# Optimization experiments

Hardware: AMD Instinct MI355X
Metric: run time of the kernel (lower is better)

The kernel has to match this reference:

```python
import jax, jax.numpy as jnp
import numpy as np

EMBED_DIM = 1024
NUM_HEADS = 16
HEAD_DIM = EMBED_DIM // NUM_HEADS
BATCH = 2
SEQ = 2048


def setup_inputs() -> dict:
    key = jax.random.key(0)
    k_x, k_wi, k_bi, k_wo, k_bo = jax.random.split(key, 5)
    scale_in = 1.0 / np.sqrt(EMBED_DIM)
    x = jax.random.normal(k_x, (BATCH, SEQ, EMBED_DIM), dtype=jnp.float32)
    # nn.Linear stores weight [out, in]; we keep [in, out] for x @ W.
    w_in = jax.random.uniform(k_wi, (EMBED_DIM, 3 * EMBED_DIM), jnp.float32, -scale_in, scale_in)
    b_in = jax.random.uniform(k_bi, (3 * EMBED_DIM,), jnp.float32, -scale_in, scale_in)
    w_out = jax.random.uniform(k_wo, (EMBED_DIM, EMBED_DIM), jnp.float32, -scale_in, scale_in)
    b_out = jax.random.uniform(k_bo, (EMBED_DIM,), jnp.float32, -scale_in, scale_in)
    return {"x": x, "w_in": w_in, "b_in": b_in, "w_out": w_out, "b_out": b_out}


def reference(x, w_in, b_in, w_out, b_out):
    B, S, E = x.shape
    H, D = NUM_HEADS, HEAD_DIM
    inp = x @ w_in + b_in                       # [B,S,3E]
    que, key, val = jnp.split(inp, 3, axis=-1)  # each [B,S,E]
    que = que.reshape(B, S, H, D)
    key = key.reshape(B, S, H, D)
    val = val.reshape(B, S, H, D)
    scores = jnp.einsum('bshd,brhd->bhsr', que, key) * (1.0 / np.sqrt(D))
    weights = jax.nn.softmax(scores, axis=-1)   # [B,H,S,S]
    attn = jnp.einsum('bhsr,brhd->bshd', weights, val).reshape(B, S, E)
    return attn @ w_out + b_out
```

## Files before the change

kernel.cpp:

```cpp
#include <hip/hip_runtime.h>


typedef __bf16 bf16x8 __attribute__((ext_vector_type(8)));
typedef float  f32x4  __attribute__((ext_vector_type(4)));
typedef float  f32x16 __attribute__((ext_vector_type(16)));
typedef short  s16x4  __attribute__((ext_vector_type(4)));
typedef short  s16x8  __attribute__((ext_vector_type(8)));

__device__ __forceinline__ unsigned short f2b(float f) {
  unsigned u = __float_as_uint(f);
  unsigned r = u + 0x7fffu + ((u >> 16) & 1u);
  return (unsigned short)(r >> 16);
}

__device__ __forceinline__ unsigned cvt_pk_bf16(float a, float b) {
#if defined(__HIP_DEVICE_COMPILE__)
  unsigned r;
  asm("v_cvt_pk_bf16_f32 %0, %1, %2" : "=v"(r) : "v"(a), "v"(b));
  return r;
#else
  return (unsigned)f2b(a) | ((unsigned)f2b(b) << 16);
#endif
}

__device__ __forceinline__ void permlane32_swap(unsigned& a, unsigned& b) {
#if defined(__HIP_DEVICE_COMPILE__)
  asm("v_permlane32_swap_b32 %0, %1" : "+v"(a), "+v"(b));
#endif
}

__device__ __forceinline__ void gl_lds16(const void* g, void* l) {
  __builtin_amdgcn_global_load_lds(
      (__attribute__((address_space(1))) void*)g,
      (__attribute__((address_space(3))) void*)l, 16, 0, 0);
}

__device__ __forceinline__ void transpose_cast_body(
    const float* __restrict__ in, unsigned short* __restrict__ out,
    int R, int C, int bx, int by, int tid, float tile[64][65]) {
  int r0 = by * 64, c0 = bx * 64;
#pragma unroll
  for (int p = 0; p < 16; p++) {
    int i = tid + p * 256;
    int ri = i >> 6, ci = i & 63;
    tile[ri][ci] = in[(size_t)(r0 + ri) * C + c0 + ci];
  }
  __syncthreads();
#pragma unroll
  for (int p = 0; p < 16; p++) {
    int i = tid + p * 256;
    int ci = i >> 6, ri = i & 63;
    out[(size_t)(c0 + ci) * R + r0 + ri] = f2b(tile[ri][ci]);
  }
}

__global__ __launch_bounds__(256) void prep_kernel(
    const float* __restrict__ x, unsigned short* __restrict__ xb,
    const float* __restrict__ w_in, unsigned short* __restrict__ wint,
    const float* __restrict__ w_out, unsigned short* __restrict__ woutt) {
  __shared__ float tile[64][65];
  int bid = blockIdx.x, tid = threadIdx.x;
  if (bid < 4096) {
    int i = bid * 256 + tid;
    float4 v = ((const float4*)x)[i];
    ushort4 o;
    o.x = f2b(v.x); o.y = f2b(v.y); o.z = f2b(v.z); o.w = f2b(v.w);
    ((ushort4*)xb)[i] = o;
  } else if (bid < 4864) {
    int l = bid - 4096;
    transpose_cast_body(w_in, wint, 1024, 3072, l % 48, l / 48, tid, tile);
  } else {
    int l = bid - 4864;
    transpose_cast_body(w_out, woutt, 1024, 1024, l % 16, l / 16, tid, tile);
  }
}

__global__ __launch_bounds__(256) void vt_transpose_kernel(
    const unsigned short* __restrict__ qkv, unsigned short* __restrict__ vt) {
  __shared__ unsigned short tile[64][65];
  int bid = blockIdx.x;
  int st = bid & 31, h = (bid >> 5) & 15, b = bid >> 9;
  int s0 = st * 64;
  int tid = threadIdx.x;
  const unsigned short* src = qkv + (size_t)(b * 2048 + s0) * 3072 + 2048 + h * 64;
#pragma unroll
  for (int p = 0; p < 16; p++) {
    int i = tid + p * 256;
    int sr = i >> 6, d = i & 63;
    tile[sr][d] = src[(size_t)sr * 3072 + d];
  }
  __syncthreads();
  unsigned short* dst = vt + (size_t)(b * 16 + h) * 64 * 2048 + s0;
#pragma unroll
  for (int p = 0; p < 16; p++) {
    int i = tid + p * 256;
    int dr = i >> 6, sc = i & 63;
    dst[(size_t)dr * 2048 + sc] = tile[sc][dr];
  }
}

__global__ __launch_bounds__(256) void gemm_bt1(
    const unsigned short* __restrict__ A, const unsigned short* __restrict__ Bt,
    const float* __restrict__ bias, unsigned short* __restrict__ Cp,
    int M, int N, int K, int qcols, float qscale) {
  __shared__ __align__(16) unsigned short As[128 * 32];
  __shared__ __align__(16) unsigned short Bs[128 * 32];
  int tid = threadIdx.x;
  int wave = tid >> 6, lane = tid & 63;
  int m_l = lane & 15, quad = lane >> 4;
  int wm = (wave >> 1) * 64, wn = (wave & 1) * 64;
  int row = tid >> 2, kp = (tid & 3) << 3;
  const unsigned short* ag = A + (size_t)(blockIdx.y * 128 + row) * K + kp;
  const unsigned short* bg = Bt + (size_t)(blockIdx.x * 128 + row) * K + kp;
  unsigned short* asw = As + wave * 512;
  unsigned short* bsw = Bs + wave * 512;
  f32x4 acc[4][4] = {};
  for (int k0 = 0; k0 < K; k0 += 32) {
    __syncthreads();
    gl_lds16(ag + k0, asw);
    gl_lds16(ag + (size_t)64 * K + k0, asw + 2048);
    gl_lds16(bg + k0, bsw);
    gl_lds16(bg + (size_t)64 * K + k0, bsw + 2048);
    __syncthreads();
    bf16x8 af[4], bf[4];
#pragma unroll
    for (int i = 0; i < 4; i++)
      af[i] = *(const bf16x8*)&As[(wm + i * 16 + m_l) * 32 + quad * 8];
#pragma unroll
    for (int j = 0; j < 4; j++)
      bf[j] = *(const bf16x8*)&Bs[(wn + j * 16 + m_l) * 32 + quad * 8];
#pragma unroll
    for (int i = 0; i < 4; i++)
#pragma unroll
      for (int j = 0; j < 4; j++)
        acc[i][j] = __builtin_amdgcn_mfma_f32_16x16x32_bf16(af[i], bf[j], acc[i][j], 0, 0, 0);
  }
  float bv[4];
#pragma unroll
  for (int j = 0; j < 4; j++) bv[j] = bias[blockIdx.x * 128 + wn + j * 16 + m_l];
#pragma unroll
  for (int i = 0; i < 4; i++) {
    int m = blockIdx.y * 128 + wm + i * 16 + quad * 4;
#pragma unroll
    for (int j = 0; j < 4; j++) {
      int n = blockIdx.x * 128 + wn + j * 16 + m_l;
      float sc = (n < qcols) ? qscale : 1.0f;
#pragma unroll
      for (int r = 0; r < 4; r++) {
        float v = (acc[i][j][r] + bv[j]) * sc;
        Cp[(size_t)(m + r) * N + n] = f2b(v);
      }
    }
  }
}

__global__ __launch_bounds__(256) void gemm_bt2(
    const unsigned short* __restrict__ A, const unsigned short* __restrict__ Bt,
    const float* __restrict__ bias, float* __restrict__ Cp, int M, int N, int K) {
  __shared__ __align__(16) unsigned short As[128 * 32];
  __shared__ __align__(16) unsigned short Bs[64 * 32];
  int tid = threadIdx.x;
  int wave = tid >> 6, lane = tid & 63;
  int m_l = lane & 15, quad = lane >> 4;
  int wm = (wave >> 1) * 64, wn = (wave & 1) * 32;
  int row = tid >> 2, kp = (tid & 3) << 3;
  const unsigned short* ag = A + (size_t)(blockIdx.y * 128 + row) * K + kp;
  const unsigned short* bg = Bt + (size_t)(blockIdx.x * 64 + row) * K + kp;
  unsigned short* asw = As + wave * 512;
  unsigned short* bsw = Bs + wave * 512;
  f32x4 acc[4][2] = {};
  for (int k0 = 0; k0 < K; k0 += 32) {
    __syncthreads();
    gl_lds16(ag + k0, asw);
    gl_lds16(ag + (size_t)64 * K + k0, asw + 2048);
    gl_lds16(bg + k0, bsw);
    __syncthreads();
    bf16x8 af[4], bf[2];
#pragma unroll
    for (int i = 0; i < 4; i++)
      af[i] = *(const bf16x8*)&As[(wm + i * 16 + m_l) * 32 + quad * 8];
#pragma unroll
    for (int j = 0; j < 2; j++)
      bf[j] = *(const bf16x8*)&Bs[(wn + j * 16 + m_l) * 32 + quad * 8];
#pragma unroll
    for (int i = 0; i < 4; i++)
#pragma unroll
      for (int j = 0; j < 2; j++)
        acc[i][j] = __builtin_amdgcn_mfma_f32_16x16x32_bf16(af[i], bf[j], acc[i][j], 0, 0, 0);
  }
  float bv[2];
#pragma unroll
  for (int j = 0; j < 2; j++) bv[j] = bias[blockIdx.x * 64 + wn + j * 16 + m_l];
#pragma unroll
  for (int i = 0; i < 4; i++) {
    int m = blockIdx.y * 128 + wm + i * 16 + quad * 4;
#pragma unroll
    for (int j = 0; j < 2; j++) {
      int n = blockIdx.x * 64 + wn + j * 16 + m_l;
#pragma unroll
      for (int r = 0; r < 4; r++)
        Cp[(size_t)(m + r) * N + n] = acc[i][j][r] + bv[j];
    }
  }
}

__global__ __launch_bounds__(256) void attn_kernel(
    const unsigned short* __restrict__ qkv, const unsigned short* __restrict__ vt,
    unsigned short* __restrict__ aout) {
  __shared__ __align__(16) unsigned short Qs[128 * 64];
  __shared__ __align__(16) unsigned short Ks[64 * 64];
  __shared__ __align__(16) unsigned short Vts[64 * 64];
  int bid = blockIdx.x;
  int qt = bid & 15, h = (bid >> 4) & 15, b = bid >> 8;
  int tid = threadIdx.x, wave = tid >> 6, lane = tid & 63;
  int l31 = lane & 31, hi = lane >> 5, l7 = lane & 7;
  int q0 = qt * 128;
  const unsigned short* qb = qkv + (size_t)b * 2048 * 3072 + h * 64;
  const unsigned short* kb = qb + 1024;
  const unsigned short* vtb = vt + (size_t)(b * 16 + h) * 64 * 2048;

  int srow = tid >> 3;
  int sd0 = ((tid & 7) ^ (srow & 7)) * 8;

#pragma unroll
  for (int p = 0; p < 4; p++)
    gl_lds16(qb + (size_t)(q0 + p * 32 + srow) * 3072 + sd0, Qs + p * 2048 + wave * 512);
  __syncthreads();

  bf16x8 qf[4];
  int qrow = (wave * 32 + l31) * 64;
#pragma unroll
  for (int ks = 0; ks < 4; ks++)
    qf[ks] = *(const bf16x8*)&Qs[qrow + ((2 * ks + hi) ^ l7) * 8];

  f32x16 oacc[2] = {};
  float lsum = 0.0f;

  for (int kt = 0; kt < 2048; kt += 64) {
    __syncthreads();
#pragma unroll
    for (int p = 0; p < 2; p++) {
      gl_lds16(kb + (size_t)(kt + p * 32 + srow) * 3072 + sd0, Ks + p * 2048 + wave * 512);
      gl_lds16(vtb + (size_t)(p * 32 + srow) * 2048 + kt + sd0, Vts + p * 2048 + wave * 512);
    }
    __syncthreads();

#pragma unroll
    for (int tt = 0; tt < 2; tt++) {
      f32x16 sacc = {};
#pragma unroll
      for (int ks = 0; ks < 4; ks++) {
        bf16x8 kf = *(const bf16x8*)&Ks[(tt * 32 + l31) * 64 + ((2 * ks + hi) ^ l7) * 8];
        sacc = __builtin_amdgcn_mfma_f32_32x32x16_bf16(kf, qf[ks], sacc, 0, 0, 0);
      }
      float pv[16];
#pragma unroll
      for (int i = 0; i < 16; i++) {
        pv[i] = __builtin_exp2f(sacc[i]);
        lsum += pv[i];
      }
#pragma unroll
      for (int g = 0; g < 2; g++) {
        unsigned a0 = cvt_pk_bf16(pv[8 * g + 0], pv[8 * g + 1]);
        unsigned a1 = cvt_pk_bf16(pv[8 * g + 2], pv[8 * g + 3]);
        unsigned b0 = cvt_pk_bf16(pv[8 * g + 4], pv[8 * g + 5]);
        unsigned b1 = cvt_pk_bf16(pv[8 * g + 6], pv[8 * g + 7]);
        permlane32_swap(a0, b0);
        permlane32_swap(a1, b1);
        union { unsigned u[4]; bf16x8 v; } pf;
        pf.u[0] = a0; pf.u[1] = a1; pf.u[2] = b0; pf.u[3] = b1;
        int kc = tt * 2 + g;
#pragma unroll
        for (int dt = 0; dt < 2; dt++) {
          bf16x8 vf = *(const bf16x8*)&Vts[(dt * 32 + l31) * 64 + ((kc * 2 + hi) ^ l7) * 8];
          oacc[dt] = __builtin_amdgcn_mfma_f32_32x32x16_bf16(vf, pf.v, oacc[dt], 0, 0, 0);
        }
      }
    }
  }

  float lp = lsum + __shfl_xor(lsum, 32, 64);
  float rl = 1.0f / lp;

  unsigned short* ob = aout + (size_t)(b * 2048 + q0 + wave * 32 + l31) * 1024 + h * 64;
#pragma unroll
  for (int dt = 0; dt < 2; dt++)
#pragma unroll
    for (int rq = 0; rq < 4; rq++) {
      union { uint2 u; ushort4 w; } pk;
      pk.u.x = cvt_pk_bf16(oacc[dt][4 * rq + 0] * rl, oacc[dt][4 * rq + 1] * rl);
      pk.u.y = cvt_pk_bf16(oacc[dt][4 * rq + 2] * rl, oacc[dt][4 * rq + 3] * rl);
      *(ushort4*)&ob[dt * 32 + rq * 8 + hi * 4] = pk.w;
    }
}

extern "C" void kernel_launch(void* const* d_in, const int* in_sizes, int n_in,
                              void* d_out, int out_size, void* d_ws, size_t ws_size,
                              hipStream_t stream) {
  (void)in_sizes; (void)n_in; (void)out_size; (void)ws_size;
  const float* x     = (const float*)d_in[0];
  const float* w_in  = (const float*)d_in[1];
  const float* b_in  = (const float*)d_in[2];
  const float* w_out = (const float*)d_in[3];
  const float* b_out = (const float*)d_in[4];
  char* ws = (char*)d_ws;
  unsigned short* xb    = (unsigned short*)(ws + 0);
  unsigned short* wint  = (unsigned short*)(ws + 8388608);
  unsigned short* woutt = (unsigned short*)(ws + 14680064);
  unsigned short* qkv   = (unsigned short*)(ws + 16777216);
  unsigned short* vt    = (unsigned short*)(ws + 41943040);
  unsigned short* attn  = (unsigned short*)(ws + 50331648);
  float* out = (float*)d_out;

  const float QSCALE = 0.125f * 1.44269504088896f;

  prep_kernel<<<5120, 256, 0, stream>>>(x, xb, w_in, wint, w_out, woutt);
  gemm_bt1<<<dim3(24, 32), 256, 0, stream>>>(xb, wint, b_in, qkv, 4096, 3072, 1024,
                                             1024, QSCALE);
  vt_transpose_kernel<<<1024, 256, 0, stream>>>(qkv, vt);
  attn_kernel<<<512, 256, 0, stream>>>(qkv, vt, attn);
  gemm_bt2<<<dim3(16, 32), 256, 0, stream>>>(attn, woutt, b_out, out, 4096, 1024, 1024);
}
```

Baseline: 212.8 us.

## Split attention KV loop across two wave groups with LDS reduction and MFMA row sums

The attention block grows to 512 threads. Each group of four waves handles half of every 128-key tile, which doubles the waves available to hide latency per block, and the two partial outputs are combined through LDS at the end. The row-sum of exp values is now computed by an MFMA against a ones vector instead of scalar adds. The cost is an extra reduction phase, more LDS per block, and bf16 rounding in the denominator sum.

```diff
diff --git a/kernel.cpp b/kernel.cpp
--- a/kernel.cpp
+++ b/kernel.cpp
@@ -204,16 +204,20 @@
   }
 }
 
-__global__ __launch_bounds__(256) void attn_kernel(
+__global__ __launch_bounds__(512, 4) void attn_kernel(
     const unsigned short* __restrict__ qkv, const unsigned short* __restrict__ vt,
     unsigned short* __restrict__ aout) {
-  __shared__ __align__(16) unsigned short Qs[128 * 64];
-  __shared__ __align__(16) unsigned short Ks[64 * 64];
-  __shared__ __align__(16) unsigned short Vts[64 * 64];
+  __shared__ __align__(16) unsigned short smem[24576];
+  unsigned short* Qs  = smem;
+  unsigned short* Ks  = smem + 8192;
+  unsigned short* Vts = smem + 16384;
+
   int bid = blockIdx.x;
   int qt = bid & 15, h = (bid >> 4) & 15, b = bid >> 8;
   int tid = threadIdx.x, wave = tid >> 6, lane = tid & 63;
   int l31 = lane & 31, hi = lane >> 5, l7 = lane & 7;
+  int w03 = wave & 3;
+  int koff = (wave >> 2) * 64;
   int q0 = qt * 128;
   const unsigned short* qb = qkv + (size_t)b * 2048 * 3072 + h * 64;
   const unsigned short* kb = qb + 1024;
@@ -221,28 +225,33 @@
 
   int srow = tid >> 3;
   int sd0 = ((tid & 7) ^ (srow & 7)) * 8;
-
-#pragma unroll
-  for (int p = 0; p < 4; p++)
-    gl_lds16(qb + (size_t)(q0 + p * 32 + srow) * 3072 + sd0, Qs + p * 2048 + wave * 512);
+  int dv = tid >> 4;
+  int sv = tid & 15;
+  int gv = (sv & 8) | ((sv & 7) ^ (dv & 7));
+
+#pragma unroll
+  for (int p = 0; p < 2; p++)
+    gl_lds16(qb + (size_t)(q0 + p * 64 + srow) * 3072 + sd0, Qs + p * 4096 + wave * 512);
   __syncthreads();
 
   bf16x8 qf[4];
-  int qrow = (wave * 32 + l31) * 64;
+  int qrow = (w03 * 32 + l31) * 64;
 #pragma unroll
   for (int ks = 0; ks < 4; ks++)
     qf[ks] = *(const bf16x8*)&Qs[qrow + ((2 * ks + hi) ^ l7) * 8];
 
+  union { s16x8 s; bf16x8 v; } onesu;
+  onesu.s = (s16x8){0x3F80, 0x3F80, 0x3F80, 0x3F80, 0x3F80, 0x3F80, 0x3F80, 0x3F80};
+
   f32x16 oacc[2] = {};
-  float lsum = 0.0f;
-
-  for (int kt = 0; kt < 2048; kt += 64) {
-    __syncthreads();
-#pragma unroll
-    for (int p = 0; p < 2; p++) {
-      gl_lds16(kb + (size_t)(kt + p * 32 + srow) * 3072 + sd0, Ks + p * 2048 + wave * 512);
-      gl_lds16(vtb + (size_t)(p * 32 + srow) * 2048 + kt + sd0, Vts + p * 2048 + wave * 512);
-    }
+  f32x16 lacc = {};
+
+  for (int kt = 0; kt < 2048; kt += 128) {
+    __syncthreads();
+    gl_lds16(kb + (size_t)(kt + srow) * 3072 + sd0, Ks + wave * 512);
+    gl_lds16(kb + (size_t)(kt + 64 + srow) * 3072 + sd0, Ks + 4096 + wave * 512);
+    gl_lds16(vtb + (size_t)dv * 2048 + kt + gv * 8, Vts + wave * 512);
+    gl_lds16(vtb + (size_t)(32 + dv) * 2048 + kt + gv * 8, Vts + 4096 + wave * 512);
     __syncthreads();
 
 #pragma unroll
@@ -250,15 +259,12 @@
       f32x16 sacc = {};
 #pragma unroll
       for (int ks = 0; ks < 4; ks++) {
-        bf16x8 kf = *(const bf16x8*)&Ks[(tt * 32 + l31) * 64 + ((2 * ks + hi) ^ l7) * 8];
+        bf16x8 kf = *(const bf16x8*)&Ks[(koff + tt * 32 + l31) * 64 + ((2 * ks + hi) ^ l7) * 8];
         sacc = __builtin_amdgcn_mfma_f32_32x32x16_bf16(kf, qf[ks], sacc, 0, 0, 0);
       }
       float pv[16];
 #pragma unroll
-      for (int i = 0; i < 16; i++) {
-        pv[i] = __builtin_exp2f(sacc[i]);
-        lsum += pv[i];
-      }
+      for (int i = 0; i < 16; i++) pv[i] = __builtin_exp2f(sacc[i]);
 #pragma unroll
       for (int g = 0; g < 2; g++) {
         unsigned a0 = cvt_pk_bf16(pv[8 * g + 0], pv[8 * g + 1]);
@@ -269,29 +275,59 @@
         permlane32_swap(a1, b1);
         union { unsigned u[4]; bf16x8 v; } pf;
         pf.u[0] = a0; pf.u[1] = a1; pf.u[2] = b0; pf.u[3] = b1;
+        lacc = __builtin_amdgcn_mfma_f32_32x32x16_bf16(onesu.v, pf.v, lacc, 0, 0, 0);
         int kc = tt * 2 + g;
 #pragma unroll
         for (int dt = 0; dt < 2; dt++) {
-          bf16x8 vf = *(const bf16x8*)&Vts[(dt * 32 + l31) * 64 + ((kc * 2 + hi) ^ l7) * 8];
+          bf16x8 vf = *(const bf16x8*)&Vts[(dt * 32 + l31) * 128 +
+                                           ((koff >> 3) | ((kc * 2 + hi) ^ l7)) * 8];
           oacc[dt] = __builtin_amdgcn_mfma_f32_32x32x16_bf16(vf, pf.v, oacc[dt], 0, 0, 0);
         }
       }
     }
   }
 
-  float lp = lsum + __shfl_xor(lsum, 32, 64);
-  float rl = 1.0f / lp;
-
-  unsigned short* ob = aout + (size_t)(b * 2048 + q0 + wave * 32 + l31) * 1024 + h * 64;
-#pragma unroll
-  for (int dt = 0; dt < 2; dt++)
-#pragma unroll
-    for (int rq = 0; rq < 4; rq++) {
-      union { uint2 u; ushort4 w; } pk;
-      pk.u.x = cvt_pk_bf16(oacc[dt][4 * rq + 0] * rl, oacc[dt][4 * rq + 1] * rl);
-      pk.u.y = cvt_pk_bf16(oacc[dt][4 * rq + 2] * rl, oacc[dt][4 * rq + 3] * rl);
-      *(ushort4*)&ob[dt * 32 + rq * 8 + hi * 4] = pk.w;
-    }
+  __syncthreads();
+  float* red = (float*)smem;
+  float* lpred = red + 8192;
+  if (wave >= 4) {
+    float* basep = red + w03 * 2048;
+#pragma unroll
+    for (int dt = 0; dt < 2; dt++)
+#pragma unroll
+      for (int r = 0; r < 4; r++) {
+        f32x4 c4 = {oacc[dt][4 * r + 0], oacc[dt][4 * r + 1],
+                    oacc[dt][4 * r + 2], oacc[dt][4 * r + 3]};
+        ((f32x4*)basep)[lane * 8 + ((dt * 4 + r) ^ (lane & 7))] = c4;
+      }
+    lpred[w03 * 64 + lane] = lacc[0];
+  }
+  __syncthreads();
+  if (wave < 4) {
+    float* basep = red + w03 * 2048;
+#pragma unroll
+    for (int dt = 0; dt < 2; dt++)
+#pragma unroll
+      for (int r = 0; r < 4; r++) {
+        f32x4 c4 = ((f32x4*)basep)[lane * 8 + ((dt * 4 + r) ^ (lane & 7))];
+        oacc[dt][4 * r + 0] += c4[0];
+        oacc[dt][4 * r + 1] += c4[1];
+        oacc[dt][4 * r + 2] += c4[2];
+        oacc[dt][4 * r + 3] += c4[3];
+      }
+    float rl = 1.0f / (lacc[0] + lpred[w03 * 64 + lane]);
+
+    unsigned short* ob = aout + (size_t)(b * 2048 + q0 + w03 * 32 + l31) * 1024 + h * 64;
+#pragma unroll
+    for (int dt = 0; dt < 2; dt++)
+#pragma unroll
+      for (int rq = 0; rq < 4; rq++) {
+        union { uint2 u; ushort4 w; } pk;
+        pk.u.x = cvt_pk_bf16(oacc[dt][4 * rq + 0] * rl, oacc[dt][4 * rq + 1] * rl);
+        pk.u.y = cvt_pk_bf16(oacc[dt][4 * rq + 2] * rl, oacc[dt][4 * rq + 3] * rl);
+        *(ushort4*)&ob[dt * 32 + rq * 8 + hi * 4] = pk.w;
+      }
+  }
 }
 
 extern "C" void kernel_launch(void* const* d_in, const int* in_sizes, int n_in,
@@ -318,6 +354,6 @@
   gemm_bt1<<<dim3(24, 32), 256, 0, stream>>>(xb, wint, b_in, qkv, 4096, 3072, 1024,
                                              1024, QSCALE);
   vt_transpose_kernel<<<1024, 256, 0, stream>>>(qkv, vt);
-  attn_kernel<<<512, 256, 0, stream>>>(qkv, vt, attn);
+  attn_kernel<<<512, 512, 0, stream>>>(qkv, vt, attn);
   gemm_bt2<<<dim3(16, 32), 256, 0, stream>>>(attn, woutt, b_out, out, 4096, 1024, 1024);
 }
```

Result: faster. 202.8 us (-4.7%).
